# Optimization experiments

Hardware: AMD Instinct MI355X
Metric: run time of the kernel (lower is better)

The kernel has to match this reference:

```python
import jax, jax.numpy as jnp
import numpy as np

N_PARTS = 4
HIDDEN = 256
NUM_FREQS = 10
IN_DIM = 3
EMB_DIM = IN_DIM * (1 + 2 * NUM_FREQS)  # 63
PART_DIM = HIDDEN // N_PARTS


def _embed(x):
    freqs = 2.0 ** jnp.arange(NUM_FREQS, dtype=x.dtype)        # [F]
    xf = x[..., None, :] * freqs[:, None]                      # [..., F, 3]
    enc = jnp.stack([jnp.sin(xf), jnp.cos(xf)], axis=-2)       # [..., F, 2, 3]
    enc = enc.reshape(x.shape[:-1] + (NUM_FREQS * 2 * IN_DIM,))
    return jnp.concatenate([x, enc], axis=-1)                  # [..., 63]


def _masks():
    # contiguous 0/1 per-part neuron masks over the HIDDEN axis (ClassMaskCreator)
    m = np.zeros((N_PARTS, HIDDEN), dtype=np.float32)
    for p in range(N_PARTS):
        s = p * PART_DIM
        e = HIDDEN if p == N_PARTS - 1 else s + PART_DIM
        m[p, s:e] = 1.0
    return jnp.asarray(m)


def setup_inputs() -> dict:
    key = jax.random.key(0)
    ks = jax.random.split(key, 8)
    B, N = 1, 131072

    def lin(k, fan_in, fan_out):
        return jax.random.normal(k, (fan_in, fan_out), jnp.float32) / np.float32(np.sqrt(fan_in))

    return {
        "coords": jax.random.normal(ks[0], (B, N, IN_DIM), jnp.float32),
        "W0": lin(ks[1], EMB_DIM, HIDDEN), "b0": jnp.zeros((HIDDEN,), jnp.float32),
        "W1": lin(ks[2], HIDDEN, HIDDEN), "b1": jnp.zeros((HIDDEN,), jnp.float32),
        "W2": lin(ks[3], HIDDEN, HIDDEN), "b2": jnp.zeros((HIDDEN,), jnp.float32),
        "Wocc": lin(ks[4], HIDDEN, 1), "bocc": jnp.zeros((1,), jnp.float32),
        "Wc": jax.random.normal(ks[5], (N_PARTS, HIDDEN), jnp.float32) / np.float32(np.sqrt(HIDDEN)),
        "bc": jnp.zeros((N_PARTS,), jnp.float32),
    }


def reference(coords, W0, b0, W1, b1, W2, b2, Wocc, bocc, Wc, bc):
    masks = _masks()                                  # [P, H]
    x = _embed(coords) @ W0 + b0                      # [B, N, H]  (no activation after layer 0, per source)

    # occupancy trunk: relu(L1) -> relu(L2) -> occ head
    x_occ = jax.nn.relu(x @ W1 + b1)
    x_occ = jax.nn.relu(x_occ @ W2 + b2)
    occ = x_occ @ Wocc + bocc                         # [B, N, 1]

    # part branches. Loop iteration i=0 masks x; i=1 indexes temporal_part_output[1*part_id],
    # i.e. the i=0 outputs. The i=1 outputs (h2) are dead w.r.t. all returned values because
    # part_features[part_id] for part_id in 0..P-1 selects the first P (i=0) entries.
    h1 = [jax.nn.relu((x * masks[p]) @ W1 + b1) for p in range(N_PARTS)]  # [B, N, H] each

    # class heads: class_heads[p](h1[p] * mask_p).squeeze(0), concatenated on last dim
    cls = [jnp.squeeze((h1[p] * masks[p]) @ Wc[p][:, None] + bc[p], axis=0)
           for p in range(N_PARTS)]                   # [N, 1] each (B == 1)
    part_class = jnp.concatenate(cls, axis=-1)        # [N, P]

    return occ, part_class
```

## Files before the change

kernel.cpp:

```cpp
#include <hip/hip_runtime.h>


#define NPTS 131072
#define M_PB 128
#define AST 264

typedef _Float16 half8   __attribute__((ext_vector_type(8)));
typedef _Float16 half4_t __attribute__((ext_vector_type(4)));
typedef float    float4_t __attribute__((ext_vector_type(4)));

__global__ void prep(const float* __restrict__ W0, const float* __restrict__ W1,
                     const float* __restrict__ W2, _Float16* __restrict__ ws) {
  int id = blockIdx.x * 256 + threadIdx.x;
  _Float16 v;
  if (id < 16384) {
    int e = id, j = e & 7, l = (e >> 3) & 63, kb = (e >> 9) & 1, tt = e >> 10;
    int c = l & 15, q = l >> 4;
    int k = kb * 32 + q * 8 + j, n = tt * 16 + c;
    v = (k < 63) ? (_Float16)W0[k * 256 + n] : (_Float16)0.f;
  } else if (id < 81920) {
    int e = id - 16384, j = e & 7, l = (e >> 3) & 63, kb = (e >> 9) & 7, tt = e >> 12;
    int c = l & 15, q = l >> 4;
    int k = kb * 32 + q * 8 + j, n = tt * 16 + c;
    v = (_Float16)W1[k * 256 + n];
  } else {
    int e = id - 81920, j = e & 7, l = (e >> 3) & 63, kb = (e >> 9) & 7, tt = e >> 12;
    int c = l & 15, q = l >> 4;
    int k = kb * 32 + q * 8 + j, n = tt * 16 + c;
    v = (_Float16)W2[k * 256 + n];
  }
  ws[id] = v;
}

template<int TOTAL_KB, int KB>
__device__ __forceinline__ void run_gemm(const _Float16* __restrict__ wb,
                                         const _Float16* __restrict__ ap,
                                         float4_t (&acc)[4][8]) {
  half8 a0[4], a1[4];
#pragma unroll
  for (int tn = 0; tn < 4; ++tn) a0[tn] = *(const half8*)(wb + tn * (TOTAL_KB * 512));
  if (KB > 1) {
#pragma unroll
    for (int tn = 0; tn < 4; ++tn) a1[tn] = *(const half8*)(wb + tn * (TOTAL_KB * 512) + 512);
  }
#pragma unroll
  for (int kb = 0; kb < KB; ++kb) {
    half8 b[8];
#pragma unroll
    for (int tm = 0; tm < 8; ++tm) b[tm] = *(const half8*)(ap + tm * 16 * AST + kb * 32);
    half8 an[4];
    if (kb + 2 < KB) {
#pragma unroll
      for (int tn = 0; tn < 4; ++tn)
        an[tn] = *(const half8*)(wb + tn * (TOTAL_KB * 512) + (kb + 2) * 512);
    }
#pragma unroll
    for (int tn = 0; tn < 4; ++tn) {
      half8 acur = (kb & 1) ? a1[tn] : a0[tn];
#pragma unroll
      for (int tm = 0; tm < 8; ++tm)
        acc[tn][tm] = __builtin_amdgcn_mfma_f32_16x16x32_f16(acur, b[tm], acc[tn][tm], 0, 0, 0);
    }
    if (kb + 2 < KB) {
#pragma unroll
      for (int tn = 0; tn < 4; ++tn) {
        if (kb & 1) a1[tn] = an[tn]; else a0[tn] = an[tn];
      }
    }
  }
}

__global__ __launch_bounds__(256, 2) void mlp_main(
    const float* __restrict__ coords,
    const _Float16* __restrict__ W0sw,
    const _Float16* __restrict__ W1sw,
    const _Float16* __restrict__ W2sw,
    const float* __restrict__ b0, const float* __restrict__ b1,
    const float* __restrict__ b2,
    const float* __restrict__ Wocc, const float* __restrict__ bocc,
    const float* __restrict__ Wc, const float* __restrict__ bc,
    float* __restrict__ out) {
  __shared__ _Float16 actX[M_PB * AST];
  __shared__ float occ_s[4][M_PB];

  const int t = threadIdx.x;
  const int w = t >> 6;
  const int l = t & 63;
  const int c = l & 15;
  const int q = l >> 4;
  const int m0 = blockIdx.x * M_PB;

  {
    int m = t & 127, kh = (t >> 7) * 32;
    const float* cp = coords + (size_t)(m0 + m) * 3;
    float x0 = cp[0], x1 = cp[1], x2 = cp[2];
#pragma unroll
    for (int i = 0; i < 4; ++i) {
      half8 ev;
#pragma unroll
      for (int u = 0; u < 8; ++u) {
        int k = kh + i * 8 + u;
        float v;
        if (k >= 63) v = 0.f;
        else if (k < 3) v = (k == 0) ? x0 : (k == 1 ? x1 : x2);
        else {
          int kk = k - 3;
          int f = kk / 6;
          int rem = kk - 6 * f;
          int s = (rem >= 3) ? 1 : 0;
          int i3 = rem - 3 * s;
          float xi = (i3 == 0) ? x0 : (i3 == 1 ? x1 : x2);
          float arg = xi * (float)(1 << f);
          float nn = rintf(arg * 0.15915494309189535f);
          float r = fmaf(nn, -6.28318548202514648f, arg);
          r = fmaf(nn, 1.7484555e-7f, r);
          v = s ? __cosf(r) : __sinf(r);
        }
        ev[u] = (_Float16)v;
      }
      *(half8*)&actX[m * AST + kh + i * 8] = ev;
    }
  }
  __syncthreads();

  float4_t acc[4][8];
  const float4_t zero4 = {0.f, 0.f, 0.f, 0.f};
  const _Float16* apc = actX + c * AST + q * 8;

#pragma unroll
  for (int tn = 0; tn < 4; ++tn)
#pragma unroll
    for (int tm = 0; tm < 8; ++tm) acc[tn][tm] = zero4;
  run_gemm<2, 2>(W0sw + (w * 4) * 2 * 512 + l * 8, apc, acc);
  __syncthreads();
#pragma unroll
  for (int tn = 0; tn < 4; ++tn) {
    float4_t bias = *(const float4_t*)(b0 + 64 * w + tn * 16 + q * 4);
#pragma unroll
    for (int tm = 0; tm < 8; ++tm) {
      float4_t v = acc[tn][tm];
      half4_t hv;
#pragma unroll
      for (int r = 0; r < 4; ++r) hv[r] = (_Float16)(v[r] + bias[r]);
      *(half4_t*)&actX[(tm * 16 + c) * AST + 64 * w + tn * 16 + q * 4] = hv;
    }
  }
  __syncthreads();

#pragma unroll
  for (int tn = 0; tn < 4; ++tn)
#pragma unroll
    for (int tm = 0; tm < 8; ++tm) acc[tn][tm] = zero4;
  run_gemm<8, 2>(W1sw + ((w * 4) * 8 + 2 * w) * 512 + l * 8, apc + 64 * w, acc);
  {
    float pcls[8] = {0.f, 0.f, 0.f, 0.f, 0.f, 0.f, 0.f, 0.f};
#pragma unroll
    for (int tn = 0; tn < 4; ++tn) {
      float4_t bias = *(const float4_t*)(b1 + 64 * w + tn * 16 + q * 4);
      float4_t wcv = *(const float4_t*)(Wc + 256 * w + 64 * w + tn * 16 + q * 4);
#pragma unroll
      for (int tm = 0; tm < 8; ++tm) {
        float4_t v = acc[tn][tm];
#pragma unroll
        for (int r = 0; r < 4; ++r) pcls[tm] += fmaxf(v[r] + bias[r], 0.f) * wcv[r];
      }
    }
    float bcw = bc[w];
#pragma unroll
    for (int tm = 0; tm < 8; ++tm) {
      float s = pcls[tm];
      s += __shfl_xor(s, 16, 64);
      s += __shfl_xor(s, 32, 64);
      if (l < 16)
        out[(size_t)NPTS + (size_t)(m0 + tm * 16 + c) * 4 + w] = s + bcw;
    }
  }

#pragma unroll
  for (int tn = 0; tn < 4; ++tn)
#pragma unroll
    for (int tm = 0; tm < 8; ++tm) acc[tn][tm] = zero4;
  run_gemm<8, 8>(W1sw + (w * 4) * 8 * 512 + l * 8, apc, acc);
  __syncthreads();
#pragma unroll
  for (int tn = 0; tn < 4; ++tn) {
    float4_t bias = *(const float4_t*)(b1 + 64 * w + tn * 16 + q * 4);
#pragma unroll
    for (int tm = 0; tm < 8; ++tm) {
      float4_t v = acc[tn][tm];
      half4_t hv;
#pragma unroll
      for (int r = 0; r < 4; ++r) hv[r] = (_Float16)fmaxf(v[r] + bias[r], 0.f);
      *(half4_t*)&actX[(tm * 16 + c) * AST + 64 * w + tn * 16 + q * 4] = hv;
    }
  }
  __syncthreads();

#pragma unroll
  for (int tn = 0; tn < 4; ++tn)
#pragma unroll
    for (int tm = 0; tm < 8; ++tm) acc[tn][tm] = zero4;
  run_gemm<8, 8>(W2sw + (w * 4) * 8 * 512 + l * 8, apc, acc);
  {
    float pocc[8] = {0.f, 0.f, 0.f, 0.f, 0.f, 0.f, 0.f, 0.f};
#pragma unroll
    for (int tn = 0; tn < 4; ++tn) {
      float4_t bias = *(const float4_t*)(b2 + 64 * w + tn * 16 + q * 4);
      float4_t wov = *(const float4_t*)(Wocc + 64 * w + tn * 16 + q * 4);
#pragma unroll
      for (int tm = 0; tm < 8; ++tm) {
        float4_t v = acc[tn][tm];
#pragma unroll
        for (int r = 0; r < 4; ++r) pocc[tm] += fmaxf(v[r] + bias[r], 0.f) * wov[r];
      }
    }
#pragma unroll
    for (int tm = 0; tm < 8; ++tm) {
      float s = pocc[tm];
      s += __shfl_xor(s, 16, 64);
      s += __shfl_xor(s, 32, 64);
      if (l < 16) occ_s[w][tm * 16 + c] = s;
    }
  }
  __syncthreads();
  if (t < M_PB) {
    out[m0 + t] = occ_s[0][t] + occ_s[1][t] + occ_s[2][t] + occ_s[3][t] + bocc[0];
  }
}

extern "C" void kernel_launch(void* const* d_in, const int* in_sizes, int n_in,
                              void* d_out, int out_size, void* d_ws, size_t ws_size,
                              hipStream_t stream) {
  const float* coords = (const float*)d_in[0];
  const float* W0   = (const float*)d_in[1];
  const float* b0   = (const float*)d_in[2];
  const float* W1   = (const float*)d_in[3];
  const float* b1   = (const float*)d_in[4];
  const float* W2   = (const float*)d_in[5];
  const float* b2   = (const float*)d_in[6];
  const float* Wocc = (const float*)d_in[7];
  const float* bocc = (const float*)d_in[8];
  const float* Wc   = (const float*)d_in[9];
  const float* bc   = (const float*)d_in[10];
  float* out = (float*)d_out;

  _Float16* ws = (_Float16*)d_ws;
  _Float16* W0sw = ws;
  _Float16* W1sw = ws + 16384;
  _Float16* W2sw = ws + 81920;

  prep<<<576, 256, 0, stream>>>(W0, W1, W2, ws);
  mlp_main<<<NPTS / M_PB, 256, 0, stream>>>(coords, W0sw, W1sw, W2sw,
                                            b0, b1, b2, Wocc, bocc, Wc, bc, out);
}
```

Before: 121.3 us.

## Halve point tile, reuse part-branch L1 partial sums for full L1, bias-init accumulators

Shrinks each block to 64 points and raises the occupancy hint to 4 blocks per SM, so accumulator registers drop from 4x8 to 4x4 tiles. The part-class layer-1 GEMM is folded into the full layer-1 GEMM: the K loop visits each wave's own two k-blocks first, reads the class-head partial at that point, then finishes the remaining six. This removes the separate 2-k-block GEMM per wave. Biases are loaded straight into the accumulators instead of being added in the epilogue, and conversions use packed cvt_pkrtz, which rounds toward zero and may shift results slightly.

```diff
diff --git a/kernel.cpp b/kernel.cpp
--- a/kernel.cpp
+++ b/kernel.cpp
@@ -2,11 +2,12 @@
 
 
 #define NPTS 131072
-#define M_PB 128
+#define M_PB 64
 #define AST 264
 
 typedef _Float16 half8   __attribute__((ext_vector_type(8)));
 typedef _Float16 half4_t __attribute__((ext_vector_type(4)));
+typedef __fp16   fp16x2  __attribute__((ext_vector_type(2)));
 typedef float    float4_t __attribute__((ext_vector_type(4)));
 
 __global__ void prep(const float* __restrict__ W0, const float* __restrict__ W1,
@@ -32,45 +33,16 @@
   ws[id] = v;
 }
 
-template<int TOTAL_KB, int KB>
-__device__ __forceinline__ void run_gemm(const _Float16* __restrict__ wb,
-                                         const _Float16* __restrict__ ap,
-                                         float4_t (&acc)[4][8]) {
-  half8 a0[4], a1[4];
-#pragma unroll
-  for (int tn = 0; tn < 4; ++tn) a0[tn] = *(const half8*)(wb + tn * (TOTAL_KB * 512));
-  if (KB > 1) {
-#pragma unroll
-    for (int tn = 0; tn < 4; ++tn) a1[tn] = *(const half8*)(wb + tn * (TOTAL_KB * 512) + 512);
-  }
-#pragma unroll
-  for (int kb = 0; kb < KB; ++kb) {
-    half8 b[8];
-#pragma unroll
-    for (int tm = 0; tm < 8; ++tm) b[tm] = *(const half8*)(ap + tm * 16 * AST + kb * 32);
-    half8 an[4];
-    if (kb + 2 < KB) {
-#pragma unroll
-      for (int tn = 0; tn < 4; ++tn)
-        an[tn] = *(const half8*)(wb + tn * (TOTAL_KB * 512) + (kb + 2) * 512);
-    }
-#pragma unroll
-    for (int tn = 0; tn < 4; ++tn) {
-      half8 acur = (kb & 1) ? a1[tn] : a0[tn];
-#pragma unroll
-      for (int tm = 0; tm < 8; ++tm)
-        acc[tn][tm] = __builtin_amdgcn_mfma_f32_16x16x32_f16(acur, b[tm], acc[tn][tm], 0, 0, 0);
-    }
-    if (kb + 2 < KB) {
-#pragma unroll
-      for (int tn = 0; tn < 4; ++tn) {
-        if (kb & 1) a1[tn] = an[tn]; else a0[tn] = an[tn];
-      }
-    }
-  }
-}
-
-__global__ __launch_bounds__(256, 2) void mlp_main(
+__device__ __forceinline__ half4_t pack4(float a, float b, float cc, float d) {
+  fp16x2 p0 = __builtin_amdgcn_cvt_pkrtz(a, b);
+  fp16x2 p1 = __builtin_amdgcn_cvt_pkrtz(cc, d);
+  half4_t h;
+  h[0] = (_Float16)p0[0]; h[1] = (_Float16)p0[1];
+  h[2] = (_Float16)p1[0]; h[3] = (_Float16)p1[1];
+  return h;
+}
+
+__global__ __launch_bounds__(256, 4) void mlp_main(
     const float* __restrict__ coords,
     const _Float16* __restrict__ W0sw,
     const _Float16* __restrict__ W1sw,
@@ -91,131 +63,198 @@
   const int m0 = blockIdx.x * M_PB;
 
   {
-    int m = t & 127, kh = (t >> 7) * 32;
-    const float* cp = coords + (size_t)(m0 + m) * 3;
+    const float* cp = coords + (size_t)(m0 + l) * 3;
     float x0 = cp[0], x1 = cp[1], x2 = cp[2];
-#pragma unroll
-    for (int i = 0; i < 4; ++i) {
-      half8 ev;
-#pragma unroll
-      for (int u = 0; u < 8; ++u) {
-        int k = kh + i * 8 + u;
-        float v;
-        if (k >= 63) v = 0.f;
-        else if (k < 3) v = (k == 0) ? x0 : (k == 1 ? x1 : x2);
-        else {
-          int kk = k - 3;
-          int f = kk / 6;
-          int rem = kk - 6 * f;
-          int s = (rem >= 3) ? 1 : 0;
-          int i3 = rem - 3 * s;
-          float xi = (i3 == 0) ? x0 : (i3 == 1 ? x1 : x2);
-          float arg = xi * (float)(1 << f);
-          float nn = rintf(arg * 0.15915494309189535f);
-          float r = fmaf(nn, -6.28318548202514648f, arg);
-          r = fmaf(nn, 1.7484555e-7f, r);
-          v = s ? __cosf(r) : __sinf(r);
+    float v[16];
+#pragma unroll
+    for (int u = 0; u < 16; ++u) {
+      int k = 16 * w + u;
+      float r;
+      if (k >= 63) r = 0.f;
+      else if (k < 3) r = (k == 0) ? x0 : (k == 1 ? x1 : x2);
+      else {
+        int kk = k - 3;
+        int f = kk / 6;
+        int rem = kk - 6 * f;
+        int s = (rem >= 3) ? 1 : 0;
+        int i3 = rem - 3 * s;
+        float xi = (i3 == 0) ? x0 : (i3 == 1 ? x1 : x2);
+        float arg = xi * (float)(1 << f);
+        float nn = rintf(arg * 0.15915494309189535f);
+        float rr = fmaf(nn, -6.28318548202514648f, arg);
+        rr = fmaf(nn, 1.7484555e-7f, rr);
+        r = s ? __cosf(rr) : __sinf(rr);
+      }
+      v[u] = r;
+    }
+    half8 e0, e1;
+#pragma unroll
+    for (int u = 0; u < 4; ++u) {
+      fp16x2 p = __builtin_amdgcn_cvt_pkrtz(v[2 * u], v[2 * u + 1]);
+      e0[2 * u] = (_Float16)p[0]; e0[2 * u + 1] = (_Float16)p[1];
+      fp16x2 p2 = __builtin_amdgcn_cvt_pkrtz(v[8 + 2 * u], v[9 + 2 * u]);
+      e1[2 * u] = (_Float16)p2[0]; e1[2 * u + 1] = (_Float16)p2[1];
+    }
+    *(half8*)&actX[l * AST + 16 * w] = e0;
+    *(half8*)&actX[l * AST + 16 * w + 8] = e1;
+  }
+  __syncthreads();
+
+  float4_t acc[4][4];
+  const _Float16* ap = actX + c * AST + q * 8;
+
+  {
+    const _Float16* wb = W0sw + (size_t)(w * 4) * 1024 + l * 8;
+    half8 a0[4], a1[4];
+#pragma unroll
+    for (int tn = 0; tn < 4; ++tn) {
+      a0[tn] = *(const half8*)(wb + tn * 1024);
+      a1[tn] = *(const half8*)(wb + tn * 1024 + 512);
+    }
+#pragma unroll
+    for (int tn = 0; tn < 4; ++tn) {
+      float4_t bz = *(const float4_t*)(b0 + 64 * w + tn * 16 + q * 4);
+#pragma unroll
+      for (int tm = 0; tm < 4; ++tm) acc[tn][tm] = bz;
+    }
+#pragma unroll
+    for (int kb = 0; kb < 2; ++kb) {
+      half8 b[4];
+#pragma unroll
+      for (int tm = 0; tm < 4; ++tm) b[tm] = *(const half8*)(ap + tm * 16 * AST + kb * 32);
+#pragma unroll
+      for (int tn = 0; tn < 4; ++tn)
+#pragma unroll
+        for (int tm = 0; tm < 4; ++tm)
+          acc[tn][tm] = __builtin_amdgcn_mfma_f32_16x16x32_f16(
+              kb ? a1[tn] : a0[tn], b[tm], acc[tn][tm], 0, 0, 0);
+    }
+  }
+  __syncthreads();
+#pragma unroll
+  for (int tn = 0; tn < 4; ++tn)
+#pragma unroll
+    for (int tm = 0; tm < 4; ++tm) {
+      float4_t v = acc[tn][tm];
+      *(half4_t*)&actX[(tm * 16 + c) * AST + 64 * w + tn * 16 + q * 4] =
+          pack4(v[0], v[1], v[2], v[3]);
+    }
+  __syncthreads();
+
+  {
+    const _Float16* wb = W1sw + (size_t)(w * 4) * 4096 + l * 8;
+    const int w2 = 2 * w;
+    float bcw = bc[w];
+#pragma unroll
+    for (int tn = 0; tn < 4; ++tn) {
+      float4_t bz = *(const float4_t*)(b1 + 64 * w + tn * 16 + q * 4);
+#pragma unroll
+      for (int tm = 0; tm < 4; ++tm) acc[tn][tm] = bz;
+    }
+    auto kbof = [&](int j) {
+      return (j < 2) ? (w2 + j) : ((j - 2) + ((j - 2) >= w2 ? 2 : 0));
+    };
+    half8 a[4], an[4];
+#pragma unroll
+    for (int tn = 0; tn < 4; ++tn) a[tn] = *(const half8*)(wb + tn * 4096 + kbof(0) * 512);
+#pragma unroll
+    for (int j = 0; j < 8; ++j) {
+      const int kb = kbof(j);
+      half8 b[4];
+#pragma unroll
+      for (int tm = 0; tm < 4; ++tm) b[tm] = *(const half8*)(ap + tm * 16 * AST + kb * 32);
+      if (j + 1 < 8) {
+        const int kbn = kbof(j + 1);
+#pragma unroll
+        for (int tn = 0; tn < 4; ++tn) an[tn] = *(const half8*)(wb + tn * 4096 + kbn * 512);
+      }
+#pragma unroll
+      for (int tn = 0; tn < 4; ++tn)
+#pragma unroll
+        for (int tm = 0; tm < 4; ++tm)
+          acc[tn][tm] = __builtin_amdgcn_mfma_f32_16x16x32_f16(a[tn], b[tm], acc[tn][tm], 0, 0, 0);
+      if (j == 1) {
+        float pcls[4] = {0.f, 0.f, 0.f, 0.f};
+#pragma unroll
+        for (int tn = 0; tn < 4; ++tn) {
+          float4_t wcv = *(const float4_t*)(Wc + 256 * w + 64 * w + tn * 16 + q * 4);
+#pragma unroll
+          for (int tm = 0; tm < 4; ++tm) {
+            float4_t v = acc[tn][tm];
+#pragma unroll
+            for (int r = 0; r < 4; ++r) pcls[tm] += fmaxf(v[r], 0.f) * wcv[r];
+          }
         }
-        ev[u] = (_Float16)v;
-      }
-      *(half8*)&actX[m * AST + kh + i * 8] = ev;
-    }
-  }
-  __syncthreads();
-
-  float4_t acc[4][8];
-  const float4_t zero4 = {0.f, 0.f, 0.f, 0.f};
-  const _Float16* apc = actX + c * AST + q * 8;
-
+#pragma unroll
+        for (int tm = 0; tm < 4; ++tm) {
+          float s = pcls[tm];
+          s += __shfl_xor(s, 16, 64);
+          s += __shfl_xor(s, 32, 64);
+          if (l < 16)
+            out[(size_t)NPTS + (size_t)(m0 + tm * 16 + c) * 4 + w] = s + bcw;
+        }
+      }
+      if (j + 1 < 8) {
+#pragma unroll
+        for (int tn = 0; tn < 4; ++tn) a[tn] = an[tn];
+      }
+    }
+  }
+  __syncthreads();
 #pragma unroll
   for (int tn = 0; tn < 4; ++tn)
 #pragma unroll
-    for (int tm = 0; tm < 8; ++tm) acc[tn][tm] = zero4;
-  run_gemm<2, 2>(W0sw + (w * 4) * 2 * 512 + l * 8, apc, acc);
-  __syncthreads();
-#pragma unroll
-  for (int tn = 0; tn < 4; ++tn) {
-    float4_t bias = *(const float4_t*)(b0 + 64 * w + tn * 16 + q * 4);
-#pragma unroll
-    for (int tm = 0; tm < 8; ++tm) {
+    for (int tm = 0; tm < 4; ++tm) {
       float4_t v = acc[tn][tm];
-      half4_t hv;
-#pragma unroll
-      for (int r = 0; r < 4; ++r) hv[r] = (_Float16)(v[r] + bias[r]);
-      *(half4_t*)&actX[(tm * 16 + c) * AST + 64 * w + tn * 16 + q * 4] = hv;
-    }
-  }
-  __syncthreads();
-
-#pragma unroll
-  for (int tn = 0; tn < 4; ++tn)
-#pragma unroll
-    for (int tm = 0; tm < 8; ++tm) acc[tn][tm] = zero4;
-  run_gemm<8, 2>(W1sw + ((w * 4) * 8 + 2 * w) * 512 + l * 8, apc + 64 * w, acc);
-  {
-    float pcls[8] = {0.f, 0.f, 0.f, 0.f, 0.f, 0.f, 0.f, 0.f};
-#pragma unroll
-    for (int tn = 0; tn < 4; ++tn) {
-      float4_t bias = *(const float4_t*)(b1 + 64 * w + tn * 16 + q * 4);
-      float4_t wcv = *(const float4_t*)(Wc + 256 * w + 64 * w + tn * 16 + q * 4);
-#pragma unroll
-      for (int tm = 0; tm < 8; ++tm) {
+      *(half4_t*)&actX[(tm * 16 + c) * AST + 64 * w + tn * 16 + q * 4] =
+          pack4(fmaxf(v[0], 0.f), fmaxf(v[1], 0.f), fmaxf(v[2], 0.f), fmaxf(v[3], 0.f));
+    }
+  __syncthreads();
+
+  {
+    const _Float16* wb = W2sw + (size_t)(w * 4) * 4096 + l * 8;
+#pragma unroll
+    for (int tn = 0; tn < 4; ++tn) {
+      float4_t bz = *(const float4_t*)(b2 + 64 * w + tn * 16 + q * 4);
+#pragma unroll
+      for (int tm = 0; tm < 4; ++tm) acc[tn][tm] = bz;
+    }
+    half8 a[4], an[4];
+#pragma unroll
+    for (int tn = 0; tn < 4; ++tn) a[tn] = *(const half8*)(wb + tn * 4096);
+#pragma unroll
+    for (int kb = 0; kb < 8; ++kb) {
+      half8 b[4];
+#pragma unroll
+      for (int tm = 0; tm < 4; ++tm) b[tm] = *(const half8*)(ap + tm * 16 * AST + kb * 32);
+      if (kb + 1 < 8) {
+#pragma unroll
+        for (int tn = 0; tn < 4; ++tn)
+          an[tn] = *(const half8*)(wb + tn * 4096 + (kb + 1) * 512);
+      }
+#pragma unroll
+      for (int tn = 0; tn < 4; ++tn)
+#pragma unroll
+        for (int tm = 0; tm < 4; ++tm)
+          acc[tn][tm] = __builtin_amdgcn_mfma_f32_16x16x32_f16(a[tn], b[tm], acc[tn][tm], 0, 0, 0);
+      if (kb + 1 < 8) {
+#pragma unroll
+        for (int tn = 0; tn < 4; ++tn) a[tn] = an[tn];
+      }
+    }
+    float pocc[4] = {0.f, 0.f, 0.f, 0.f};
+#pragma unroll
+    for (int tn = 0; tn < 4; ++tn) {
+      float4_t wov = *(const float4_t*)(Wocc + 64 * w + tn * 16 + q * 4);
+#pragma unroll
+      for (int tm = 0; tm < 4; ++tm) {
         float4_t v = acc[tn][tm];
 #pragma unroll
-        for (int r = 0; r < 4; ++r) pcls[tm] += fmaxf(v[r] + bias[r], 0.f) * wcv[r];
-      }
-    }
-    float bcw = bc[w];
-#pragma unroll
-    for (int tm = 0; tm < 8; ++tm) {
-      float s = pcls[tm];
-      s += __shfl_xor(s, 16, 64);
-      s += __shfl_xor(s, 32, 64);
-      if (l < 16)
-        out[(size_t)NPTS + (size_t)(m0 + tm * 16 + c) * 4 + w] = s + bcw;
-    }
-  }
-
-#pragma unroll
-  for (int tn = 0; tn < 4; ++tn)
-#pragma unroll
-    for (int tm = 0; tm < 8; ++tm) acc[tn][tm] = zero4;
-  run_gemm<8, 8>(W1sw + (w * 4) * 8 * 512 + l * 8, apc, acc);
-  __syncthreads();
-#pragma unroll
-  for (int tn = 0; tn < 4; ++tn) {
-    float4_t bias = *(const float4_t*)(b1 + 64 * w + tn * 16 + q * 4);
-#pragma unroll
-    for (int tm = 0; tm < 8; ++tm) {
-      float4_t v = acc[tn][tm];
-      half4_t hv;
-#pragma unroll
-      for (int r = 0; r < 4; ++r) hv[r] = (_Float16)fmaxf(v[r] + bias[r], 0.f);
-      *(half4_t*)&actX[(tm * 16 + c) * AST + 64 * w + tn * 16 + q * 4] = hv;
-    }
-  }
-  __syncthreads();
-
-#pragma unroll
-  for (int tn = 0; tn < 4; ++tn)
-#pragma unroll
-    for (int tm = 0; tm < 8; ++tm) acc[tn][tm] = zero4;
-  run_gemm<8, 8>(W2sw + (w * 4) * 8 * 512 + l * 8, apc, acc);
-  {
-    float pocc[8] = {0.f, 0.f, 0.f, 0.f, 0.f, 0.f, 0.f, 0.f};
-#pragma unroll
-    for (int tn = 0; tn < 4; ++tn) {
-      float4_t bias = *(const float4_t*)(b2 + 64 * w + tn * 16 + q * 4);
-      float4_t wov = *(const float4_t*)(Wocc + 64 * w + tn * 16 + q * 4);
-#pragma unroll
-      for (int tm = 0; tm < 8; ++tm) {
-        float4_t v = acc[tn][tm];
-#pragma unroll
-        for (int r = 0; r < 4; ++r) pocc[tm] += fmaxf(v[r] + bias[r], 0.f) * wov[r];
-      }
-    }
-#pragma unroll
-    for (int tm = 0; tm < 8; ++tm) {
+        for (int r = 0; r < 4; ++r) pocc[tm] += fmaxf(v[r], 0.f) * wov[r];
+      }
+    }
+#pragma unroll
+    for (int tm = 0; tm < 4; ++tm) {
       float s = pocc[tm];
       s += __shfl_xor(s, 16, 64);
       s += __shfl_xor(s, 32, 64);
```

After: 126.5 us. 4.3% more time.
